# Optimization experiments

Hardware: AMD Instinct MI355X
Metric: run time of the kernel (lower is better)

Reference implementation:

```python
import jax, jax.numpy as jnp
import numpy as np


def setup_inputs() -> dict:
    key = jax.random.key(0)
    k1, k2 = jax.random.split(key)
    B, L, J, N = 8, 32, 128, 512
    ypred = jax.random.normal(k1, (B, L, J, N), dtype=jnp.float32)
    xyz = jax.random.normal(k2, (B, L, N, 3), dtype=jnp.float32)
    return {"ypred": ypred, "xyz": xyz}


def _pairwise_dist(x):
    # x: [BL, N, 3] -> Euclidean distance [BL, N, N] via the mm trick,
    # with the diagonal forced to exactly 0 (matching torch.cdist(x, x)).
    sq = jnp.sum(x * x, axis=-1)                       # [BL, N]
    d2 = sq[:, :, None] + sq[:, None, :] - 2.0 * jnp.einsum('bnd,bmd->bnm', x, x)
    d2 = jnp.maximum(d2, 0.0)
    dist = jnp.sqrt(d2)
    n = x.shape[1]
    eye = jnp.eye(n, dtype=bool)
    return jnp.where(eye[None, :, :], 0.0, dist)


def reference(ypred, xyz):
    B, L, J, N = ypred.shape
    x = xyz.reshape(B * L, N, 3)
    dist = _pairwise_dist(x)                           # [BL, N, N]
    max_idx = jnp.argmax(dist, axis=2)                 # [BL, N] farthest point
    dist_masked = jnp.where(dist == 0.0, 1e6, dist)    # mask self (and exact dupes)
    min_idx = jnp.argmin(dist_masked, axis=2)          # [BL, N] nearest point

    # per-point logit vectors: [BL, N, J]
    yp = jnp.transpose(ypred, (0, 1, 3, 2)).reshape(B * L, N, J)
    sim = jnp.einsum('bnj,bmj->bnm', yp, yp)           # [BL, N, N]

    sim_at_max = jnp.take_along_axis(sim, max_idx[:, :, None], axis=2)[..., 0]
    sim_at_min = jnp.take_along_axis(sim, min_idx[:, :, None], axis=2)[..., 0]
    return jnp.mean(sim_at_max - sim_at_min)
```

## Files before the change

kernel.cpp:

```cpp
#include <hip/hip_runtime.h>

#pragma clang fp contract(off)

#define NBATCH 256
#define NPTS   512
#define JDIM   128
#define NPAIR  (NBATCH * NPTS)

__global__ __launch_bounds__(512) void argmm_kernel(
    const float* __restrict__ xyz,
    int* __restrict__ pmax,
    int* __restrict__ pmin)
{
    __shared__ float4 xyzS[NPTS];
    __shared__ float mv[16][128];  __shared__ int mi[16][128];
    __shared__ float nv[16][128];  __shared__ int ni[16][128];

    const int t  = threadIdx.x;
    const int bl = blockIdx.x >> 2;
    const int qq = blockIdx.x & 3;
    const float* xp = xyz + (size_t)bl * NPTS * 3;

    {
        float x = xp[3 * t], y = xp[3 * t + 1], z = xp[3 * t + 2];
        float sq = (x * x + y * y) + z * z;
        xyzS[t] = make_float4(-2.0f * x, -2.0f * y, -2.0f * z, sq);
    }

    const int g = t & 31, s = t >> 5;
    const int pbase = qq * 128 + g * 4;
    float ox[4], oy[4], oz[4], oq[4];
    {
        const float4* own = (const float4*)(xp + 3 * pbase);
        float4 o0 = own[0], o1 = own[1], o2 = own[2];
        ox[0] = o0.x; oy[0] = o0.y; oz[0] = o0.z;
        ox[1] = o0.w; oy[1] = o1.x; oz[1] = o1.y;
        ox[2] = o1.z; oy[2] = o1.w; oz[2] = o2.x;
        ox[3] = o2.y; oy[3] = o2.z; oz[3] = o2.w;
        #pragma unroll
        for (int k = 0; k < 4; ++k)
            oq[k] = (ox[k] * ox[k] + oy[k] * oy[k]) + oz[k] * oz[k];
    }
    __syncthreads();

    const int mbase = s * 32;
    float bmax[4], bmin[4]; int ima[4], imi[4];
    #pragma unroll
    for (int k = 0; k < 4; ++k) {
        bmax[k] = -1.0f; bmin[k] = 3.0e38f; ima[k] = mbase; imi[k] = mbase;
    }

    #pragma unroll 8
    for (int mm = 0; mm < 32; ++mm) {
        int m = mbase + mm;
        float4 qv = xyzS[m];
        #pragma unroll
        for (int k = 0; k < 4; ++k) {
            float dt = (ox[k] * qv.x + oy[k] * qv.y) + oz[k] * qv.z;
            float d2 = (oq[k] + qv.w) + dt;
            bool gt = d2 > bmax[k];
            ima[k] = gt ? m : ima[k];  bmax[k] = gt ? d2 : bmax[k];
            bool lt = (d2 < bmin[k]) && (d2 > 0.0f);
            imi[k] = lt ? m : imi[k];  bmin[k] = lt ? d2 : bmin[k];
        }
    }

    #pragma unroll
    for (int k = 0; k < 4; ++k) {
        int pt = g * 4 + k;
        mv[s][pt] = bmax[k];  mi[s][pt] = ima[k];
        nv[s][pt] = bmin[k];  ni[s][pt] = imi[k];
    }
    __syncthreads();

    if (t < 256) {
        const int pt = t & 127;
        const int out_idx = bl * NPTS + qq * 128 + pt;
        if (t < 128) {
            float bv = mv[0][pt]; int bi = mi[0][pt];
            #pragma unroll
            for (int ss = 1; ss < 16; ++ss) {
                float v = mv[ss][pt]; int i = mi[ss][pt];
                bool w = v > bv; bi = w ? i : bi; bv = w ? v : bv;
            }
            pmax[out_idx] = bi;
        } else {
            float sv = nv[0][pt]; int si = ni[0][pt];
            #pragma unroll
            for (int ss = 1; ss < 16; ++ss) {
                float u = nv[ss][pt]; int j = ni[ss][pt];
                bool x = u < sv; si = x ? j : si; sv = x ? u : sv;
            }
            pmin[out_idx] = si;
        }
    }
}

__global__ __launch_bounds__(512) void sim_kernel(
    const float* __restrict__ ypred,
    const int* __restrict__ pmax,
    const int* __restrict__ pmin,
    float* __restrict__ partials)
{
    __shared__ float L[16 * NPTS];
    __shared__ float wred[8];

    const int t  = threadIdx.x;
    const int bl = blockIdx.x >> 3;
    const int c  = blockIdx.x & 7;

    const int pma = pmax[bl * NPTS + t];
    const int pmi = pmin[bl * NPTS + t];

    const float4* src = (const float4*)(ypred + (size_t)bl * JDIM * NPTS
                                              + (size_t)c * 16 * NPTS);
    float4 v0 = src[t], v1 = src[512 + t], v2 = src[1024 + t], v3 = src[1536 + t];
    float4* dst = (float4*)L;
    dst[t] = v0;  dst[512 + t] = v1;  dst[1024 + t] = v2;  dst[1536 + t] = v3;
    __syncthreads();

    float accP = 0.0f, accM = 0.0f;
    #pragma unroll
    for (int r = 0; r < 16; ++r) {
        float a  = L[r * NPTS + t];
        float b  = L[r * NPTS + pma];
        float cm = L[r * NPTS + pmi];
        accP = fmaf(a, b, accP);
        accM = fmaf(a, cm, accM);
    }

    float d = accP - accM;
    #pragma unroll
    for (int off = 32; off > 0; off >>= 1)
        d += __shfl_down(d, off);
    if ((t & 63) == 0) wred[t >> 6] = d;
    __syncthreads();
    if (t == 0) {
        float ssum = 0.0f;
        #pragma unroll
        for (int w = 0; w < 8; ++w) ssum += wred[w];
        partials[blockIdx.x] = ssum;
    }
}

__global__ __launch_bounds__(1024) void reduce_mean_kernel(
    const float* __restrict__ partials, float* __restrict__ out)
{
    const int t = threadIdx.x;
    float v = partials[t] + partials[t + 1024];
    #pragma unroll
    for (int off = 32; off > 0; off >>= 1)
        v += __shfl_down(v, off);

    __shared__ float w[16];
    if ((t & 63) == 0) w[t >> 6] = v;
    __syncthreads();
    if (t == 0) {
        float s = 0.0f;
        #pragma unroll
        for (int i = 0; i < 16; ++i) s += w[i];
        out[0] = s * (1.0f / (float)NPAIR);
    }
}

extern "C" void kernel_launch(void* const* d_in, const int* in_sizes, int n_in,
                              void* d_out, int out_size, void* d_ws, size_t ws_size,
                              hipStream_t stream) {
    const float* ypred = (const float*)d_in[0];
    const float* xyz   = (const float*)d_in[1];

    int*   pmax     = (int*)d_ws;
    int*   pmin     = pmax + NPAIR;
    float* partials = (float*)(pmin + NPAIR);
    float* out      = (float*)d_out;

    argmm_kernel<<<4 * NBATCH, 512, 0, stream>>>(xyz, pmax, pmin);
    sim_kernel<<<8 * NBATCH, 512, 0, stream>>>(ypred, pmax, pmin, partials);
    reduce_mean_kernel<<<1, 1024, 0, stream>>>(partials, out);
}
```

Before: 116.1 us.

## Fuse argmax/argmin and similarity into one per-batch kernel with prefetch pipeline

Merges the distance argmax/argmin kernel and the similarity kernel into one block per batch element. Each thread now scans all 512 points for its own point, so the nearest and farthest indices stay in registers instead of going through global memory. The ypred chunks are prefetched into registers three chunks ahead and staged in double-buffered LDS, overlapping the loads with the argmax scan and the dot products. In exchange, the grid shrinks to 256 blocks with one large-LDS block per CU, which lowers occupancy and parallelism, and each thread runs a longer serial scan.

New measurement: 148.8 us. 28.1% more time.

```diff
diff --git a/kernel.cpp b/kernel.cpp
--- a/kernel.cpp
+++ b/kernel.cpp
@@ -6,141 +6,102 @@
 #define NPTS   512
 #define JDIM   128
 #define NPAIR  (NBATCH * NPTS)
+#define NCHUNK 8
+#define ROWS   16
 
-__global__ __launch_bounds__(512) void argmm_kernel(
+__global__ __launch_bounds__(512) void fused_kernel(
+    const float* __restrict__ ypred,
     const float* __restrict__ xyz,
-    int* __restrict__ pmax,
-    int* __restrict__ pmin)
+    float* __restrict__ partials)
 {
     __shared__ float4 xyzS[NPTS];
-    __shared__ float mv[16][128];  __shared__ int mi[16][128];
-    __shared__ float nv[16][128];  __shared__ int ni[16][128];
+    __shared__ __align__(16) float Lt[2][ROWS * NPTS];
+    __shared__ float wredc[NCHUNK][8];
 
     const int t  = threadIdx.x;
-    const int bl = blockIdx.x >> 2;
-    const int qq = blockIdx.x & 3;
-    const float* xp = xyz + (size_t)bl * NPTS * 3;
+    const int bl = blockIdx.x;
+    const float*  xp  = xyz + (size_t)bl * NPTS * 3;
+    const float4* src = (const float4*)(ypred + (size_t)bl * JDIM * NPTS);
+
+    float4 r0[4], r1[4], r2[4];
+    #pragma unroll
+    for (int q = 0; q < 4; ++q) r0[q] = src[0 * 2048 + q * 512 + t];
+    #pragma unroll
+    for (int q = 0; q < 4; ++q) r1[q] = src[1 * 2048 + q * 512 + t];
+    #pragma unroll
+    for (int q = 0; q < 4; ++q) r2[q] = src[2 * 2048 + q * 512 + t];
+
+    float ox = xp[3 * t], oy = xp[3 * t + 1], oz = xp[3 * t + 2];
+    float oq = (ox * ox + oy * oy) + oz * oz;
+    xyzS[t] = make_float4(-2.0f * ox, -2.0f * oy, -2.0f * oz, oq);
+    __syncthreads();
+
+    float bmax = -1.0f, bmin = 3.0e38f;
+    int   ima  = 0,     imi  = 0;
+    #pragma unroll 8
+    for (int m = 0; m < NPTS; ++m) {
+        float4 qv = xyzS[m];
+        float dt = (ox * qv.x + oy * qv.y) + oz * qv.z;
+        float d2 = (oq + qv.w) + dt;
+        bool gt = d2 > bmax;
+        ima = gt ? m : ima;  bmax = gt ? d2 : bmax;
+        bool lt = (d2 < bmin) && (d2 > 0.0f);
+        imi = lt ? m : imi;  bmin = lt ? d2 : bmin;
+    }
+    const int pma = ima, pmi = imi;
 
     {
-        float x = xp[3 * t], y = xp[3 * t + 1], z = xp[3 * t + 2];
-        float sq = (x * x + y * y) + z * z;
-        xyzS[t] = make_float4(-2.0f * x, -2.0f * y, -2.0f * z, sq);
-    }
-
-    const int g = t & 31, s = t >> 5;
-    const int pbase = qq * 128 + g * 4;
-    float ox[4], oy[4], oz[4], oq[4];
-    {
-        const float4* own = (const float4*)(xp + 3 * pbase);
-        float4 o0 = own[0], o1 = own[1], o2 = own[2];
-        ox[0] = o0.x; oy[0] = o0.y; oz[0] = o0.z;
-        ox[1] = o0.w; oy[1] = o1.x; oz[1] = o1.y;
-        ox[2] = o1.z; oy[2] = o1.w; oz[2] = o2.x;
-        ox[3] = o2.y; oy[3] = o2.z; oz[3] = o2.w;
+        float4* dst = (float4*)Lt[0];
         #pragma unroll
-        for (int k = 0; k < 4; ++k)
-            oq[k] = (ox[k] * ox[k] + oy[k] * oy[k]) + oz[k] * oz[k];
+        for (int q = 0; q < 4; ++q) dst[q * 512 + t] = r0[q];
     }
     __syncthreads();
 
-    const int mbase = s * 32;
-    float bmax[4], bmin[4]; int ima[4], imi[4];
+#define PREFETCH(cc, R)                                                        \
+    { _Pragma("unroll")                                                        \
+      for (int q = 0; q < 4; ++q) R[q] = src[(cc) * 2048 + q * 512 + t]; }
+#define DSWRITE(cc, R)                                                         \
+    { float4* dst = (float4*)Lt[(cc) & 1];                                     \
+      _Pragma("unroll")                                                        \
+      for (int q = 0; q < 4; ++q) dst[q * 512 + t] = R[q]; }
+
     #pragma unroll
-    for (int k = 0; k < 4; ++k) {
-        bmax[k] = -1.0f; bmin[k] = 3.0e38f; ima[k] = mbase; imi[k] = mbase;
-    }
-
-    #pragma unroll 8
-    for (int mm = 0; mm < 32; ++mm) {
-        int m = mbase + mm;
-        float4 qv = xyzS[m];
+    for (int c = 0; c < NCHUNK; ++c) {
+        if (c + 3 < NCHUNK) {
+            if (c % 3 == 0)      PREFETCH(c + 3, r0)
+            else if (c % 3 == 1) PREFETCH(c + 3, r1)
+            else                 PREFETCH(c + 3, r2)
+        }
+        if (c + 1 < NCHUNK) {
+            if ((c + 1) % 3 == 0)      DSWRITE(c + 1, r0)
+            else if ((c + 1) % 3 == 1) DSWRITE(c + 1, r1)
+            else                       DSWRITE(c + 1, r2)
+        }
+        const float* L = Lt[c & 1];
+        float accP = 0.0f, accM = 0.0f;
         #pragma unroll
-        for (int k = 0; k < 4; ++k) {
-            float dt = (ox[k] * qv.x + oy[k] * qv.y) + oz[k] * qv.z;
-            float d2 = (oq[k] + qv.w) + dt;
-            bool gt = d2 > bmax[k];
-            ima[k] = gt ? m : ima[k];  bmax[k] = gt ? d2 : bmax[k];
-            bool lt = (d2 < bmin[k]) && (d2 > 0.0f);
-            imi[k] = lt ? m : imi[k];  bmin[k] = lt ? d2 : bmin[k];
+        for (int r = 0; r < ROWS; ++r) {
+            float a  = L[r * NPTS + t];
+            float b  = L[r * NPTS + pma];
+            float cm = L[r * NPTS + pmi];
+            accP = fmaf(a, b, accP);
+            accM = fmaf(a, cm, accM);
+        }
+        float d = accP - accM;
+        #pragma unroll
+        for (int off = 32; off > 0; off >>= 1)
+            d += __shfl_down(d, off);
+        if ((t & 63) == 0) wredc[c][t >> 6] = d;
+        __syncthreads();
+        if (t == 0) {
+            float ssum = 0.0f;
+            #pragma unroll
+            for (int w = 0; w < 8; ++w) ssum += wredc[c][w];
+            partials[bl * NCHUNK + c] = ssum;
         }
     }
-
-    #pragma unroll
-    for (int k = 0; k < 4; ++k) {
-        int pt = g * 4 + k;
-        mv[s][pt] = bmax[k];  mi[s][pt] = ima[k];
-        nv[s][pt] = bmin[k];  ni[s][pt] = imi[k];
-    }
-    __syncthreads();
-
-    if (t < 256) {
-        const int pt = t & 127;
-        const int out_idx = bl * NPTS + qq * 128 + pt;
-        if (t < 128) {
-            float bv = mv[0][pt]; int bi = mi[0][pt];
-            #pragma unroll
-            for (int ss = 1; ss < 16; ++ss) {
-                float v = mv[ss][pt]; int i = mi[ss][pt];
-                bool w = v > bv; bi = w ? i : bi; bv = w ? v : bv;
-            }
-            pmax[out_idx] = bi;
-        } else {
-            float sv = nv[0][pt]; int si = ni[0][pt];
-            #pragma unroll
-            for (int ss = 1; ss < 16; ++ss) {
-                float u = nv[ss][pt]; int j = ni[ss][pt];
-                bool x = u < sv; si = x ? j : si; sv = x ? u : sv;
-            }
-            pmin[out_idx] = si;
-        }
-    }
-}
-
-__global__ __launch_bounds__(512) void sim_kernel(
-    const float* __restrict__ ypred,
-    const int* __restrict__ pmax,
-    const int* __restrict__ pmin,
-    float* __restrict__ partials)
-{
-    __shared__ float L[16 * NPTS];
-    __shared__ float wred[8];
-
-    const int t  = threadIdx.x;
-    const int bl = blockIdx.x >> 3;
-    const int c  = blockIdx.x & 7;
-
-    const int pma = pmax[bl * NPTS + t];
-    const int pmi = pmin[bl * NPTS + t];
-
-    const float4* src = (const float4*)(ypred + (size_t)bl * JDIM * NPTS
-                                              + (size_t)c * 16 * NPTS);
-    float4 v0 = src[t], v1 = src[512 + t], v2 = src[1024 + t], v3 = src[1536 + t];
-    float4* dst = (float4*)L;
-    dst[t] = v0;  dst[512 + t] = v1;  dst[1024 + t] = v2;  dst[1536 + t] = v3;
-    __syncthreads();
-
-    float accP = 0.0f, accM = 0.0f;
-    #pragma unroll
-    for (int r = 0; r < 16; ++r) {
-        float a  = L[r * NPTS + t];
-        float b  = L[r * NPTS + pma];
-        float cm = L[r * NPTS + pmi];
-        accP = fmaf(a, b, accP);
-        accM = fmaf(a, cm, accM);
-    }
-
-    float d = accP - accM;
-    #pragma unroll
-    for (int off = 32; off > 0; off >>= 1)
-        d += __shfl_down(d, off);
-    if ((t & 63) == 0) wred[t >> 6] = d;
-    __syncthreads();
-    if (t == 0) {
-        float ssum = 0.0f;
-        #pragma unroll
-        for (int w = 0; w < 8; ++w) ssum += wred[w];
-        partials[blockIdx.x] = ssum;
-    }
+#undef PREFETCH
+#undef DSWRITE
 }
 
 __global__ __launch_bounds__(1024) void reduce_mean_kernel(
@@ -169,12 +130,9 @@
     const float* ypred = (const float*)d_in[0];
     const float* xyz   = (const float*)d_in[1];
 
-    int*   pmax     = (int*)d_ws;
-    int*   pmin     = pmax + NPAIR;
-    float* partials = (float*)(pmin + NPAIR);
+    float* partials = (float*)d_ws;
     float* out      = (float*)d_out;
 
-    argmm_kernel<<<4 * NBATCH, 512, 0, stream>>>(xyz, pmax, pmin);
-    sim_kernel<<<8 * NBATCH, 512, 0, stream>>>(ypred, pmax, pmin, partials);
+    fused_kernel<<<NBATCH, 512, 0, stream>>>(ypred, xyz, partials);
     reduce_mean_kernel<<<1, 1024, 0, stream>>>(partials, out);
 }
```

## Assign one query point per thread in argmax/argmin kernel, drop cross-slice reduction

Applied to the files above, without the earlier changes.

The argmax/argmin kernel is reorganised so each of 128 threads scans all 512 candidate points for a single query point, instead of 512 threads each handling 4 points over a 32-candidate slice followed by a shared-memory reduction across 16 slices. This removes the large shared-memory reduction buffers, the second barrier and the merge step. In exchange each block has a quarter of the threads and each thread runs a 16x longer serial loop, which lowers per-block parallelism and latency hiding. Tie-breaking now follows a plain sequential scan.

New measurement: 125.4 us. 7.9% more time.

```diff
diff --git a/kernel.cpp b/kernel.cpp
--- a/kernel.cpp
+++ b/kernel.cpp
@@ -7,93 +7,46 @@
 #define JDIM   128
 #define NPAIR  (NBATCH * NPTS)
 
-__global__ __launch_bounds__(512) void argmm_kernel(
+__global__ __launch_bounds__(128) void argmm_kernel(
     const float* __restrict__ xyz,
     int* __restrict__ pmax,
     int* __restrict__ pmin)
 {
     __shared__ float4 xyzS[NPTS];
-    __shared__ float mv[16][128];  __shared__ int mi[16][128];
-    __shared__ float nv[16][128];  __shared__ int ni[16][128];
 
     const int t  = threadIdx.x;
     const int bl = blockIdx.x >> 2;
     const int qq = blockIdx.x & 3;
     const float* xp = xyz + (size_t)bl * NPTS * 3;
 
-    {
-        float x = xp[3 * t], y = xp[3 * t + 1], z = xp[3 * t + 2];
+    #pragma unroll
+    for (int i = 0; i < 4; ++i) {
+        int m = t + i * 128;
+        float x = xp[3 * m], y = xp[3 * m + 1], z = xp[3 * m + 2];
         float sq = (x * x + y * y) + z * z;
-        xyzS[t] = make_float4(-2.0f * x, -2.0f * y, -2.0f * z, sq);
+        xyzS[m] = make_float4(-2.0f * x, -2.0f * y, -2.0f * z, sq);
     }
 
-    const int g = t & 31, s = t >> 5;
-    const int pbase = qq * 128 + g * 4;
-    float ox[4], oy[4], oz[4], oq[4];
-    {
-        const float4* own = (const float4*)(xp + 3 * pbase);
-        float4 o0 = own[0], o1 = own[1], o2 = own[2];
-        ox[0] = o0.x; oy[0] = o0.y; oz[0] = o0.z;
-        ox[1] = o0.w; oy[1] = o1.x; oz[1] = o1.y;
-        ox[2] = o1.z; oy[2] = o1.w; oz[2] = o2.x;
-        ox[3] = o2.y; oy[3] = o2.z; oz[3] = o2.w;
-        #pragma unroll
-        for (int k = 0; k < 4; ++k)
-            oq[k] = (ox[k] * ox[k] + oy[k] * oy[k]) + oz[k] * oz[k];
-    }
+    const int p = qq * 128 + t;
+    float ox = xp[3 * p], oy = xp[3 * p + 1], oz = xp[3 * p + 2];
+    float oq = (ox * ox + oy * oy) + oz * oz;
     __syncthreads();
 
-    const int mbase = s * 32;
-    float bmax[4], bmin[4]; int ima[4], imi[4];
-    #pragma unroll
-    for (int k = 0; k < 4; ++k) {
-        bmax[k] = -1.0f; bmin[k] = 3.0e38f; ima[k] = mbase; imi[k] = mbase;
+    float bmax = -1.0f, bmin = 3.0e38f;
+    int   ima  = 0,     imi  = 0;
+    #pragma unroll 8
+    for (int m = 0; m < NPTS; ++m) {
+        float4 qv = xyzS[m];
+        float dt = (ox * qv.x + oy * qv.y) + oz * qv.z;
+        float d2 = (oq + qv.w) + dt;
+        bool gt = d2 > bmax;
+        ima = gt ? m : ima;  bmax = gt ? d2 : bmax;
+        bool lt = (d2 < bmin) && (d2 > 0.0f);
+        imi = lt ? m : imi;  bmin = lt ? d2 : bmin;
     }
 
-    #pragma unroll 8
-    for (int mm = 0; mm < 32; ++mm) {
-        int m = mbase + mm;
-        float4 qv = xyzS[m];
-        #pragma unroll
-        for (int k = 0; k < 4; ++k) {
-            float dt = (ox[k] * qv.x + oy[k] * qv.y) + oz[k] * qv.z;
-            float d2 = (oq[k] + qv.w) + dt;
-            bool gt = d2 > bmax[k];
-            ima[k] = gt ? m : ima[k];  bmax[k] = gt ? d2 : bmax[k];
-            bool lt = (d2 < bmin[k]) && (d2 > 0.0f);
-            imi[k] = lt ? m : imi[k];  bmin[k] = lt ? d2 : bmin[k];
-        }
-    }
-
-    #pragma unroll
-    for (int k = 0; k < 4; ++k) {
-        int pt = g * 4 + k;
-        mv[s][pt] = bmax[k];  mi[s][pt] = ima[k];
-        nv[s][pt] = bmin[k];  ni[s][pt] = imi[k];
-    }
-    __syncthreads();
-
-    if (t < 256) {
-        const int pt = t & 127;
-        const int out_idx = bl * NPTS + qq * 128 + pt;
-        if (t < 128) {
-            float bv = mv[0][pt]; int bi = mi[0][pt];
-            #pragma unroll
-            for (int ss = 1; ss < 16; ++ss) {
-                float v = mv[ss][pt]; int i = mi[ss][pt];
-                bool w = v > bv; bi = w ? i : bi; bv = w ? v : bv;
-            }
-            pmax[out_idx] = bi;
-        } else {
-            float sv = nv[0][pt]; int si = ni[0][pt];
-            #pragma unroll
-            for (int ss = 1; ss < 16; ++ss) {
-                float u = nv[ss][pt]; int j = ni[ss][pt];
-                bool x = u < sv; si = x ? j : si; sv = x ? u : sv;
-            }
-            pmin[out_idx] = si;
-        }
-    }
+    pmax[bl * NPTS + p] = ima;
+    pmin[bl * NPTS + p] = imi;
 }
 
 __global__ __launch_bounds__(512) void sim_kernel(
@@ -174,7 +127,7 @@
     float* partials = (float*)(pmin + NPAIR);
     float* out      = (float*)d_out;
 
-    argmm_kernel<<<4 * NBATCH, 512, 0, stream>>>(xyz, pmax, pmin);
+    argmm_kernel<<<4 * NBATCH, 128, 0, stream>>>(xyz, pmax, pmin);
     sim_kernel<<<8 * NBATCH, 512, 0, stream>>>(ypred, pmax, pmin, partials);
     reduce_mean_kernel<<<1, 1024, 0, stream>>>(partials, out);
 }
```
